# Optimization experiments

Hardware: AMD Instinct MI355X
Metric: run time of the kernel (lower is better)

Reference implementation:

```python
import jax, jax.numpy as jnp
import numpy as np

B, T, C = 2, 2048, 2048
H = 16
HD = C // H  # 128; kv_size == hidden_size so kv head dim == HD


def setup_inputs() -> dict:
    key = jax.random.key(0)
    ks = jax.random.split(key, 5)
    s = 0.02
    return {
        "x": jax.random.normal(ks[0], (B, T, C), dtype=jnp.float32),
        "Wq": jax.random.normal(ks[1], (C, C), dtype=jnp.float32) * s,
        "Wk": jax.random.normal(ks[2], (C, C), dtype=jnp.float32) * s,
        "Wv": jax.random.normal(ks[3], (C, C), dtype=jnp.float32) * s,
        "Wo": jax.random.normal(ks[4], (C, C), dtype=jnp.float32) * s,
    }


def reference(x, Wq, Wk, Wv, Wo):
    # Linear(bias=False): y = x @ W.T
    q = (x @ Wq.T).reshape(B, T, H, HD).transpose(0, 2, 1, 3)  # [B,H,T,HD]
    k = (x @ Wk.T).reshape(B, T, H, HD).transpose(0, 2, 1, 3)
    v = (x @ Wv.T).reshape(B, T, H, HD).transpose(0, 2, 1, 3)
    scale = 1.0 / np.sqrt(HD).astype(np.float32)
    att = jnp.einsum("bhqd,bhkd->bhqk", q, k) * scale  # [B,H,T,T]
    att = jax.nn.softmax(att, axis=-1)
    y = jnp.einsum("bhqk,bhkd->bhqd", att, v)  # [B,H,T,HD]
    y = y.transpose(0, 2, 1, 3).reshape(B, T, C)
    return y @ Wo.T
```

## Files before the change

### kernel.cpp

```cpp
#include <hip/hip_runtime.h>
#include <hip/hip_bf16.h>

typedef __attribute__((ext_vector_type(8))) short short8;
typedef __attribute__((ext_vector_type(4))) float f32x4;
typedef __attribute__((ext_vector_type(16))) float f32x16;
typedef unsigned short u16;
typedef unsigned int u32;

__device__ __forceinline__ u16 f2bf(float f){
  __hip_bfloat16 h = __float2bfloat16(f);
  return *reinterpret_cast<u16*>(&h);
}

__device__ __forceinline__ void gld16(const void* g, void* l){
  __builtin_amdgcn_global_load_lds((const __attribute__((address_space(1))) void*)g,
                                   (__attribute__((address_space(3))) void*)l, 16, 0, 0);
}

#define SCHED0() __builtin_amdgcn_sched_barrier(0)

__global__ __launch_bounds__(256) void cvt_kernel(const float* __restrict__ src,
                                                  u16* __restrict__ dst, int n){
  int i0 = (blockIdx.x*256 + threadIdx.x)*4;
  int stride = gridDim.x*256*4;
  for (int i = i0; i < n; i += stride){
    float4 f = *reinterpret_cast<const float4*>(src + i);
    ushort4 u;
    u.x = f2bf(f.x); u.y = f2bf(f.y); u.z = f2bf(f.z); u.w = f2bf(f.w);
    *reinterpret_cast<ushort4*>(dst + i) = u;
  }
}

__device__ __forceinline__ void gemm256_body(const u16* __restrict__ A,
    const u16* __restrict__ W, void* __restrict__ outp, float scale, int epi)
{
  __shared__ alignas(16) u16 Lds[73728];
  const int tid = threadIdx.x;
  const int w = tid>>6, l = tid&63;
  const int l15 = l&15, lg = l>>4;
  const int wm = w&1, wn = (w>>1)&1, wk = w>>2;
  const int row0 = blockIdx.y*128, col0 = blockIdx.x*256;
  constexpr int K = 2048;
  constexpr int NT = K/64;

  f32x4 acc[4][8];
  #pragma unroll
  for (int i=0;i<4;i++)
    #pragma unroll
    for (int j=0;j<8;j++)
      #pragma unroll
      for (int r=0;r<4;r++) acc[i][j][r] = 0.f;

  int sBrow[4], sBcol[4];
  #pragma unroll
  for (int p=0;p<4;p++){
    int s = p*512 + tid;
    sBrow[p] = s>>3;  sBcol[p] = ((s&7) ^ ((s>>3)&7))*8;
  }
  const int sArow0 = sBrow[0], sAcol0 = sBcol[0];
  const int sArow1 = sBrow[1], sAcol1 = sBcol[1];

  auto stageA = [&](int slot, int kt){
    gld16(A + (size_t)(row0 + sArow0)*K + kt*64 + sAcol0,
          &Lds[slot*8192 + (size_t)(w*64)*8]);
    gld16(A + (size_t)(row0 + sArow1)*K + kt*64 + sAcol1,
          &Lds[slot*8192 + (size_t)(512 + w*64)*8]);
  };
  auto stageB = [&](int slot, int kt){
    #pragma unroll
    for (int p=0;p<4;p++)
      gld16(W + (size_t)(col0 + sBrow[p])*K + kt*64 + sBcol[p],
            &Lds[24576 + slot*16384 + (size_t)(p*512 + w*64)*8]);
  };
  auto readA = [&](int slot, short8 (&af)[4]){
    #pragma unroll
    for (int i=0;i<4;i++){
      int r = wm*64 + i*16 + l15;
      int byt = slot*16384 + r*128 + (((wk*4+lg) ^ (r&7))<<4);
      af[i] = *reinterpret_cast<const short8*>((const char*)Lds + byt);
    }
  };
  auto readB = [&](int slot, short8 (&bf)[8]){
    #pragma unroll
    for (int j=0;j<8;j++){
      int r = wn*128 + j*16 + l15;
      int byt = 49152 + slot*32768 + r*128 + (((wk*4+lg) ^ (r&7))<<4);
      bf[j] = *reinterpret_cast<const short8*>((const char*)Lds + byt);
    }
  };

  stageA(0, 0); stageB(0, 0);
  stageA(1, 1); stageB(1, 1);
  SCHED0();
  asm volatile("s_waitcnt vmcnt(6)" ::: "memory");
  __builtin_amdgcn_s_barrier();
  SCHED0();

  int sl = 0;
  for (int t=0; t<NT; ++t){
    int st = sl+2; if (st>=3) st-=3;
    int tn = (t+2) & (NT-1);
    stageA(st, tn);
    stageB(st, tn);
    short8 af[4], bf[8];
    readA(sl, af);
    readB(sl, bf);
    #pragma unroll
    for (int i=0;i<4;i++)
      #pragma unroll
      for (int j=0;j<8;j++)
        acc[i][j] = __builtin_amdgcn_mfma_f32_16x16x32_bf16(af[i], bf[j], acc[i][j], 0, 0, 0);
    SCHED0();
    asm volatile("s_waitcnt vmcnt(6)" ::: "memory");
    __builtin_amdgcn_s_barrier();
    SCHED0();
    sl = sl+1; if (sl>=3) sl = 0;
  }

  __syncthreads();
  float* R = (float*)Lds;
  const int pair = wm*2 + wn;
  if (wk == 1){
    #pragma unroll
    for (int i=0;i<4;i++)
      #pragma unroll
      for (int j=0;j<8;j++)
        *reinterpret_cast<f32x4*>(&R[pair*8192 + (i*8+j)*256 + l*4]) = acc[i][j];
  }
  __syncthreads();
  if (wk == 0){
    #pragma unroll
    for (int i=0;i<4;i++)
      #pragma unroll
      for (int j=0;j<8;j++){
        f32x4 o = *reinterpret_cast<const f32x4*>(&R[pair*8192 + (i*8+j)*256 + l*4]);
        #pragma unroll
        for (int r=0;r<4;r++) acc[i][j][r] += o[r];
      }

    if (epi == 0){
      u16* O = (u16*)outp;
      #pragma unroll
      for (int i=0;i<4;i++)
        #pragma unroll
        for (int j=0;j<8;j++)
          #pragma unroll
          for (int r=0;r<4;r++){
            int m = row0 + wm*64 + i*16 + lg*4 + r;
            int n = col0 + wn*128 + j*16 + l15;
            int b = m >> 11, tt = m & 2047;
            int h = n >> 7,  d = n & 127;
            O[(((size_t)(b*16 + h)*2048 + tt)<<7) + d] = f2bf(acc[i][j][r] * scale);
          }
    } else if (epi == 2){
      u16* O = (u16*)outp;
      #pragma unroll
      for (int i=0;i<4;i++)
        #pragma unroll
        for (int j=0;j<8;j++){
          int m0 = row0 + wm*64 + i*16 + lg*4;
          int n  = col0 + wn*128 + j*16 + l15;
          int b = m0 >> 11, tt = m0 & 2047;
          int h = n >> 7,  d = n & 127;
          ushort4 u;
          u.x = f2bf(acc[i][j][0]); u.y = f2bf(acc[i][j][1]);
          u.z = f2bf(acc[i][j][2]); u.w = f2bf(acc[i][j][3]);
          *reinterpret_cast<ushort4*>(&O[(((size_t)(b*16 + h)<<7) + d)*2048 + tt]) = u;
        }
    } else {
      float* O = (float*)outp;
      #pragma unroll
      for (int i=0;i<4;i++)
        #pragma unroll
        for (int j=0;j<8;j++)
          #pragma unroll
          for (int r=0;r<4;r++){
            int m = row0 + wm*64 + i*16 + lg*4 + r;
            int n = col0 + wn*128 + j*16 + l15;
            O[(size_t)m*2048 + n] = acc[i][j][r];
          }
    }
  }
}

__global__ __launch_bounds__(512,2) void gemm_qkv(const u16* __restrict__ A,
    const u16* __restrict__ Wq, const u16* __restrict__ Wk, const u16* __restrict__ Wv,
    u16* __restrict__ qo, u16* __restrict__ ko, u16* __restrict__ vt, float qscale)
{
  const u16* W; void* O; float sc; int epi;
  if (blockIdx.z == 0){ W = Wq; O = qo; sc = qscale; epi = 0; }
  else if (blockIdx.z == 1){ W = Wk; O = ko; sc = 1.f; epi = 0; }
  else { W = Wv; O = vt; sc = 1.f; epi = 2; }
  gemm256_body(A, W, O, sc, epi);
}

__global__ __launch_bounds__(512,2) void gemm_out(const u16* __restrict__ A,
    const u16* __restrict__ W, float* __restrict__ O)
{
  gemm256_body(A, W, O, 1.f, 1);
}

__global__ __launch_bounds__(256,2) void attn_kernel(
    const u16* __restrict__ Q, const u16* __restrict__ Kg,
    const u16* __restrict__ Vt, u16* __restrict__ Y)
{
  __shared__ alignas(16) u16 Ks[2][64*128];
  __shared__ alignas(16) u16 Vs[2][64*128];
  const int tid = threadIdx.x;
  const int w = tid>>6, l = tid&63;
  const int l31 = l&31, hi = l>>5;
  const int bh_swz = ((blockIdx.x&7)*64 + (blockIdx.x>>3));
  const int bh = bh_swz >> 4;
  const int q0 = (bh_swz & 15) * 128;

  short8 qf[8];
  #pragma unroll
  for (int ds=0; ds<8; ds++)
    qf[ds] = *reinterpret_cast<const short8*>(
        Q + ((size_t)bh*2048 + q0 + w*32 + l31)*128 + ds*16 + hi*8);

  f32x16 accO[4];
  #pragma unroll
  for (int dt=0;dt<4;dt++)
    #pragma unroll
    for (int r=0;r<16;r++) accO[dt][r] = 0.f;
  float mrun = -1e30f, lrun = 0.f;

  int krow_[4], kcol_[4], vd_[4], vkv_[4];
  #pragma unroll
  for (int p=0;p<4;p++){
    int s = p*256 + tid;
    int r = s>>4, c = s&15;
    int cu = c ^ (r&15);
    krow_[p] = r;  kcol_[p] = cu*8;
    vd_[p] = r*2 + (cu>>3);  vkv_[p] = (cu&7)*8;
  }

  auto stage = [&](int buf, int kvt){
    int kv0 = kvt*64;
    #pragma unroll
    for (int p=0;p<4;p++)
      gld16(Kg + ((size_t)bh*2048 + kv0 + krow_[p])*128 + kcol_[p],
            &Ks[buf][(size_t)(p*256 + w*64)*8]);
    #pragma unroll
    for (int p=0;p<4;p++)
      gld16(Vt + ((size_t)bh*128 + vd_[p])*2048 + kv0 + vkv_[p],
            &Vs[buf][(size_t)(p*256 + w*64)*8]);
  };

  stage(0, 0);
  __syncthreads();

  int cur = 0;
  for (int kvt=0; kvt<32; ++kvt){
    if (kvt+1 < 32) stage(cur^1, kvt+1);

    f32x16 accS[2];
    #pragma unroll
    for (int kt=0;kt<2;kt++)
      #pragma unroll
      for (int r=0;r<16;r++) accS[kt][r] = 0.f;
    #pragma unroll
    for (int kt=0;kt<2;kt++){
      #pragma unroll
      for (int ds=0;ds<8;ds++){
        int row = kt*32 + l31;
        int byt = row*256 + (((ds*2 + hi) ^ (row&15))<<4);
        short8 kf = *reinterpret_cast<const short8*>((const char*)(&Ks[cur][0]) + byt);
        accS[kt] = __builtin_amdgcn_mfma_f32_32x32x16_bf16(kf, qf[ds], accS[kt], 0, 0, 0);
      }
    }

    float pmax = accS[0][0];
    #pragma unroll
    for (int kt=0;kt<2;kt++)
      #pragma unroll
      for (int r=0;r<16;r++) pmax = fmaxf(pmax, accS[kt][r]);
    pmax = fmaxf(pmax, __shfl_xor(pmax, 32, 64));
    if (__any(pmax > mrun + 8.f)){
      float mn = fmaxf(mrun, pmax);
      float c = __expf(mrun - mn);
      mrun = mn;
      lrun *= c;
      #pragma unroll
      for (int r=0;r<16;r++){
        int qrow = (r&3) + 8*(r>>2) + 4*hi;
        float cr = __shfl(c, qrow, 64);
        #pragma unroll
        for (int dt=0;dt<4;dt++) accO[dt][r] *= cr;
      }
    }

    float rs = 0.f;
    short8 pa[4];
    #pragma unroll
    for (int kt=0;kt<2;kt++){
      #pragma unroll
      for (int b=0;b<2;b++){
        float e0 = __expf(accS[kt][b*8+0] - mrun);
        float e1 = __expf(accS[kt][b*8+1] - mrun);
        float e2 = __expf(accS[kt][b*8+2] - mrun);
        float e3 = __expf(accS[kt][b*8+3] - mrun);
        float e4 = __expf(accS[kt][b*8+4] - mrun);
        float e5 = __expf(accS[kt][b*8+5] - mrun);
        float e6 = __expf(accS[kt][b*8+6] - mrun);
        float e7 = __expf(accS[kt][b*8+7] - mrun);
        rs += (e0+e1)+(e2+e3)+(e4+e5)+(e6+e7);
        u32 x01 = (u32)f2bf(e0) | ((u32)f2bf(e1)<<16);
        u32 x23 = (u32)f2bf(e2) | ((u32)f2bf(e3)<<16);
        u32 y01 = (u32)f2bf(e4) | ((u32)f2bf(e5)<<16);
        u32 y23 = (u32)f2bf(e6) | ((u32)f2bf(e7)<<16);
        u32 sx_x01 = __shfl_xor(x01, 32, 64);
        u32 sx_x23 = __shfl_xor(x23, 32, 64);
        u32 sx_y01 = __shfl_xor(y01, 32, 64);
        u32 sx_y23 = __shfl_xor(y23, 32, 64);
        int4 wv;
        wv.x = (int)(hi ? sx_y01 : x01);
        wv.y = (int)(hi ? sx_y23 : x23);
        wv.z = (int)(hi ? y01 : sx_x01);
        wv.w = (int)(hi ? y23 : sx_x23);
        pa[kt*2+b] = *reinterpret_cast<short8*>(&wv);
      }
    }
    rs += __shfl_xor(rs, 32, 64);
    lrun += rs;

    #pragma unroll
    for (int dt=0;dt<4;dt++){
      #pragma unroll
      for (int ks=0;ks<4;ks++){
        int d = dt*32 + l31;
        int cu = (d&1)*8 + ks*2 + hi;
        int byt = (d>>1)*256 + ((cu ^ ((d>>1)&15))<<4);
        short8 vf = *reinterpret_cast<const short8*>((const char*)(&Vs[cur][0]) + byt);
        accO[dt] = __builtin_amdgcn_mfma_f32_32x32x16_bf16(pa[ks], vf, accO[dt], 0, 0, 0);
      }
    }

    __syncthreads();
    cur ^= 1;
  }

  const int b_ = bh >> 4, h_ = bh & 15;
  float inv = 1.f / lrun;
  #pragma unroll
  for (int r=0;r<16;r++){
    int qrow = (r&3) + 8*(r>>2) + 4*hi;
    float lr = __shfl(inv, qrow, 64);
    int t = q0 + w*32 + qrow;
    #pragma unroll
    for (int dt=0;dt<4;dt++){
      int d = dt*32 + l31;
      Y[((size_t)b_*2048 + t)*2048 + h_*128 + d] = f2bf(accO[dt][r] * lr);
    }
  }
}

extern "C" void kernel_launch(void* const* d_in, const int* in_sizes, int n_in,
                              void* d_out, int out_size, void* d_ws, size_t ws_size,
                              hipStream_t stream)
{
  const float* x  = (const float*)d_in[0];
  const float* Wq = (const float*)d_in[1];
  const float* Wk = (const float*)d_in[2];
  const float* Wv = (const float*)d_in[3];
  const float* Wo = (const float*)d_in[4];
  float* out = (float*)d_out;
  char* ws = (char*)d_ws;

  const size_t MB = 1024*1024;
  u16* xb  = (u16*)(ws);
  u16* wqb = (u16*)(ws + 16*MB);
  u16* wkb = (u16*)(ws + 24*MB);
  u16* wvb = (u16*)(ws + 32*MB);
  u16* wob = (u16*)(ws + 40*MB);
  u16* qb  = (u16*)(ws + 48*MB);
  u16* kb  = (u16*)(ws + 64*MB);
  u16* vtb = (u16*)(ws + 80*MB);
  u16* yb  = wqb;

  cvt_kernel<<<2048, 256, 0, stream>>>(x,  xb,  4096*2048);
  cvt_kernel<<<1024, 256, 0, stream>>>(Wq, wqb, 2048*2048);
  cvt_kernel<<<1024, 256, 0, stream>>>(Wk, wkb, 2048*2048);
  cvt_kernel<<<1024, 256, 0, stream>>>(Wv, wvb, 2048*2048);
  cvt_kernel<<<1024, 256, 0, stream>>>(Wo, wob, 2048*2048);

  const float qscale = 0.08838834764831845f;
  gemm_qkv<<<dim3(8,32,3), 512, 0, stream>>>(xb, wqb, wkb, wvb, qb, kb, vtb, qscale);
  attn_kernel<<<512, 256, 0, stream>>>(qb, kb, vtb, yb);
  gemm_out<<<dim3(8,32), 512, 0, stream>>>(yb, wob, out);
}
```

Measured before the change: 265.6 us.

## Enlarge attention blocks to 256 queries, interleave softmax with PV, batch weight casts

The attention kernel now runs 512 threads per block covering 256 query rows, so each K/V tile staged in LDS is shared by eight waves instead of four and the grid halves to 256 blocks. The score, softmax and PV MFMA steps are interleaved per 32-key subtile, which lowers peak register pressure so launch bounds can ask for 4 blocks per CU. The four weight fp32-to-bf16 conversions are merged into one launch to cut launch overhead. Risks: 256 blocks may underfill the GPU's CUs, and the occupancy request may cause spills.

New measurement: 419.8 us. 58.1% more time.

```diff
diff --git a/kernel.cpp b/kernel.cpp
--- a/kernel.cpp
+++ b/kernel.cpp
@@ -28,6 +28,26 @@
     ushort4 u;
     u.x = f2bf(f.x); u.y = f2bf(f.y); u.z = f2bf(f.z); u.w = f2bf(f.w);
     *reinterpret_cast<ushort4*>(dst + i) = u;
+  }
+}
+
+__global__ __launch_bounds__(256) void cvt4_kernel(
+    const float* __restrict__ s0, const float* __restrict__ s1,
+    const float* __restrict__ s2, const float* __restrict__ s3,
+    u16* __restrict__ d0, u16* __restrict__ d1,
+    u16* __restrict__ d2, u16* __restrict__ d3, int n){
+  const float* s; u16* d;
+  if (blockIdx.y == 0){ s = s0; d = d0; }
+  else if (blockIdx.y == 1){ s = s1; d = d1; }
+  else if (blockIdx.y == 2){ s = s2; d = d2; }
+  else { s = s3; d = d3; }
+  int i0 = (blockIdx.x*256 + threadIdx.x)*4;
+  int stride = gridDim.x*256*4;
+  for (int i = i0; i < n; i += stride){
+    float4 f = *reinterpret_cast<const float4*>(s + i);
+    ushort4 u;
+    u.x = f2bf(f.x); u.y = f2bf(f.y); u.z = f2bf(f.z); u.w = f2bf(f.w);
+    *reinterpret_cast<ushort4*>(d + i) = u;
   }
 }
 
@@ -200,7 +220,7 @@
   gemm256_body(A, W, O, 1.f, 1);
 }
 
-__global__ __launch_bounds__(256,2) void attn_kernel(
+__global__ __launch_bounds__(512,4) void attn_kernel(
     const u16* __restrict__ Q, const u16* __restrict__ Kg,
     const u16* __restrict__ Vt, u16* __restrict__ Y)
 {
@@ -209,9 +229,9 @@
   const int tid = threadIdx.x;
   const int w = tid>>6, l = tid&63;
   const int l31 = l&31, hi = l>>5;
-  const int bh_swz = ((blockIdx.x&7)*64 + (blockIdx.x>>3));
-  const int bh = bh_swz >> 4;
-  const int q0 = (bh_swz & 15) * 128;
+  const int swz = (blockIdx.x&7)*32 + (blockIdx.x>>3);
+  const int bh = swz >> 3;
+  const int q0 = (swz & 7) * 256;
 
   short8 qf[8];
   #pragma unroll
@@ -226,10 +246,10 @@
     for (int r=0;r<16;r++) accO[dt][r] = 0.f;
   float mrun = -1e30f, lrun = 0.f;
 
-  int krow_[4], kcol_[4], vd_[4], vkv_[4];
-  #pragma unroll
-  for (int p=0;p<4;p++){
-    int s = p*256 + tid;
+  int krow_[2], kcol_[2], vd_[2], vkv_[2];
+  #pragma unroll
+  for (int p=0;p<2;p++){
+    int s = p*512 + tid;
     int r = s>>4, c = s&15;
     int cu = c ^ (r&15);
     krow_[p] = r;  kcol_[p] = cu*8;
@@ -239,13 +259,13 @@
   auto stage = [&](int buf, int kvt){
     int kv0 = kvt*64;
     #pragma unroll
-    for (int p=0;p<4;p++)
+    for (int p=0;p<2;p++)
       gld16(Kg + ((size_t)bh*2048 + kv0 + krow_[p])*128 + kcol_[p],
-            &Ks[buf][(size_t)(p*256 + w*64)*8]);
-    #pragma unroll
-    for (int p=0;p<4;p++)
+            &Ks[buf][(size_t)(p*512 + w*64)*8]);
+    #pragma unroll
+    for (int p=0;p<2;p++)
       gld16(Vt + ((size_t)bh*128 + vd_[p])*2048 + kv0 + vkv_[p],
-            &Vs[buf][(size_t)(p*256 + w*64)*8]);
+            &Vs[buf][(size_t)(p*512 + w*64)*8]);
   };
 
   stage(0, 0);
@@ -255,56 +275,48 @@
   for (int kvt=0; kvt<32; ++kvt){
     if (kvt+1 < 32) stage(cur^1, kvt+1);
 
-    f32x16 accS[2];
-    #pragma unroll
-    for (int kt=0;kt<2;kt++)
-      #pragma unroll
-      for (int r=0;r<16;r++) accS[kt][r] = 0.f;
     #pragma unroll
     for (int kt=0;kt<2;kt++){
+      f32x16 accS;
+      #pragma unroll
+      for (int r=0;r<16;r++) accS[r] = 0.f;
       #pragma unroll
       for (int ds=0;ds<8;ds++){
         int row = kt*32 + l31;
         int byt = row*256 + (((ds*2 + hi) ^ (row&15))<<4);
         short8 kf = *reinterpret_cast<const short8*>((const char*)(&Ks[cur][0]) + byt);
-        accS[kt] = __builtin_amdgcn_mfma_f32_32x32x16_bf16(kf, qf[ds], accS[kt], 0, 0, 0);
+        accS = __builtin_amdgcn_mfma_f32_32x32x16_bf16(kf, qf[ds], accS, 0, 0, 0);
       }
-    }
-
-    float pmax = accS[0][0];
-    #pragma unroll
-    for (int kt=0;kt<2;kt++)
-      #pragma unroll
-      for (int r=0;r<16;r++) pmax = fmaxf(pmax, accS[kt][r]);
-    pmax = fmaxf(pmax, __shfl_xor(pmax, 32, 64));
-    if (__any(pmax > mrun + 8.f)){
-      float mn = fmaxf(mrun, pmax);
-      float c = __expf(mrun - mn);
-      mrun = mn;
-      lrun *= c;
-      #pragma unroll
-      for (int r=0;r<16;r++){
-        int qrow = (r&3) + 8*(r>>2) + 4*hi;
-        float cr = __shfl(c, qrow, 64);
-        #pragma unroll
-        for (int dt=0;dt<4;dt++) accO[dt][r] *= cr;
+
+      float pmax = accS[0];
+      #pragma unroll
+      for (int r=1;r<16;r++) pmax = fmaxf(pmax, accS[r]);
+      pmax = fmaxf(pmax, __shfl_xor(pmax, 32, 64));
+      if (__any(pmax > mrun + 8.f)){
+        float mn = fmaxf(mrun, pmax);
+        float c = __expf(mrun - mn);
+        mrun = mn;
+        lrun *= c;
+        #pragma unroll
+        for (int r=0;r<16;r++){
+          int qrow = (r&3) + 8*(r>>2) + 4*hi;
+          float cr = __shfl(c, qrow, 64);
+          #pragma unroll
+          for (int dt=0;dt<4;dt++) accO[dt][r] *= cr;
+        }
       }
-    }
-
-    float rs = 0.f;
-    short8 pa[4];
-    #pragma unroll
-    for (int kt=0;kt<2;kt++){
+
+      float rs = 0.f;
       #pragma unroll
       for (int b=0;b<2;b++){
-        float e0 = __expf(accS[kt][b*8+0] - mrun);
-        float e1 = __expf(accS[kt][b*8+1] - mrun);
-        float e2 = __expf(accS[kt][b*8+2] - mrun);
-        float e3 = __expf(accS[kt][b*8+3] - mrun);
-        float e4 = __expf(accS[kt][b*8+4] - mrun);
-        float e5 = __expf(accS[kt][b*8+5] - mrun);
-        float e6 = __expf(accS[kt][b*8+6] - mrun);
-        float e7 = __expf(accS[kt][b*8+7] - mrun);
+        float e0 = __expf(accS[b*8+0] - mrun);
+        float e1 = __expf(accS[b*8+1] - mrun);
+        float e2 = __expf(accS[b*8+2] - mrun);
+        float e3 = __expf(accS[b*8+3] - mrun);
+        float e4 = __expf(accS[b*8+4] - mrun);
+        float e5 = __expf(accS[b*8+5] - mrun);
+        float e6 = __expf(accS[b*8+6] - mrun);
+        float e7 = __expf(accS[b*8+7] - mrun);
         rs += (e0+e1)+(e2+e3)+(e4+e5)+(e6+e7);
         u32 x01 = (u32)f2bf(e0) | ((u32)f2bf(e1)<<16);
         u32 x23 = (u32)f2bf(e2) | ((u32)f2bf(e3)<<16);
@@ -319,22 +331,19 @@
         wv.y = (int)(hi ? sx_y23 : x23);
         wv.z = (int)(hi ? y01 : sx_x01);
         wv.w = (int)(hi ? y23 : sx_x23);
-        pa[kt*2+b] = *reinterpret_cast<short8*>(&wv);
+        short8 pa = *reinterpret_cast<short8*>(&wv);
+        int ks = kt*2 + b;
+        #pragma unroll
+        for (int dt=0;dt<4;dt++){
+          int d = dt*32 + l31;
+          int cu = (d&1)*8 + ks*2 + hi;
+          int byt = (d>>1)*256 + ((cu ^ ((d>>1)&15))<<4);
+          short8 vf = *reinterpret_cast<const short8*>((const char*)(&Vs[cur][0]) + byt);
+          accO[dt] = __builtin_amdgcn_mfma_f32_32x32x16_bf16(pa, vf, accO[dt], 0, 0, 0);
+        }
       }
-    }
-    rs += __shfl_xor(rs, 32, 64);
-    lrun += rs;
-
-    #pragma unroll
-    for (int dt=0;dt<4;dt++){
-      #pragma unroll
-      for (int ks=0;ks<4;ks++){
-        int d = dt*32 + l31;
-        int cu = (d&1)*8 + ks*2 + hi;
-        int byt = (d>>1)*256 + ((cu ^ ((d>>1)&15))<<4);
-        short8 vf = *reinterpret_cast<const short8*>((const char*)(&Vs[cur][0]) + byt);
-        accO[dt] = __builtin_amdgcn_mfma_f32_32x32x16_bf16(pa[ks], vf, accO[dt], 0, 0, 0);
-      }
+      rs += __shfl_xor(rs, 32, 64);
+      lrun += rs;
     }
 
     __syncthreads();
@@ -379,14 +388,12 @@
   u16* vtb = (u16*)(ws + 80*MB);
   u16* yb  = wqb;
 
-  cvt_kernel<<<2048, 256, 0, stream>>>(x,  xb,  4096*2048);
-  cvt_kernel<<<1024, 256, 0, stream>>>(Wq, wqb, 2048*2048);
-  cvt_kernel<<<1024, 256, 0, stream>>>(Wk, wkb, 2048*2048);
-  cvt_kernel<<<1024, 256, 0, stream>>>(Wv, wvb, 2048*2048);
-  cvt_kernel<<<1024, 256, 0, stream>>>(Wo, wob, 2048*2048);
+  cvt_kernel<<<2048, 256, 0, stream>>>(x, xb, 4096*2048);
+  cvt4_kernel<<<dim3(1024,4), 256, 0, stream>>>(Wq, Wk, Wv, Wo,
+                                                wqb, wkb, wvb, wob, 2048*2048);
 
   const float qscale = 0.08838834764831845f;
   gemm_qkv<<<dim3(8,32,3), 512, 0, stream>>>(xb, wqb, wkb, wvb, qb, kb, vtb, qscale);
-  attn_kernel<<<512, 256, 0, stream>>>(qb, kb, vtb, yb);
+  attn_kernel<<<256, 512, 0, stream>>>(qb, kb, vtb, yb);
   gemm_out<<<dim3(8,32), 512, 0, stream>>>(yb, wob, out);
 }
```
